# Kernel tuning notes

Measured on AMD Instinct MI355X. Metric: run time of the kernel, lower is better.

Reference implementation:

```python
import jax, jax.numpy as jnp
from jax import lax
import numpy as np

HEAD_SIZE = 64
D_MIX = 32
D_DECAY = 64
D_GATE = 64


def setup_inputs() -> dict:
    key = jax.random.key(0)
    B, T, C = 4, 2048, 1024
    H = C // HEAD_SIZE
    ks = jax.random.split(key, 24)
    n = lambda i, shape, s=1.0: (jax.random.normal(ks[i], shape, dtype=jnp.float32) * s)
    return {
        "x": n(0, (B, T, C)),
        "maa_x": n(1, (C,), 0.1), "maa_w": n(2, (C,), 0.1), "maa_k": n(3, (C,), 0.1),
        "maa_v": n(4, (C,), 0.1), "maa_r": n(5, (C,), 0.1), "maa_g": n(6, (C,), 0.1),
        "maa_w1": n(7, (C, 5 * D_MIX), 0.01), "maa_w2": n(8, (5, D_MIX, C), 0.01),
        "Wr": n(9, (C, C), C ** -0.5), "Wk": n(10, (C, C), C ** -0.5),
        "Wv": n(11, (C, C), C ** -0.5), "Wo": n(12, (C, C), C ** -0.5),
        "gate_w1": n(13, (C, D_GATE), 0.01), "gate_w2": n(14, (D_GATE, C), 0.01),
        "time_decay": n(15, (C,), 1.0) - 4.0,
        "decay_w1": n(16, (C, D_DECAY), 0.01), "decay_w2": n(17, (D_DECAY, C), 0.01),
        "u": n(18, (H, HEAD_SIZE), 0.1),
        "ln_g": jnp.ones((C,), jnp.float32), "ln_b": jnp.zeros((C,), jnp.float32),
    }


def _wkv6(r, k, v, w, u):
    # r,k,v: [B,T,C]; w: decay (already exp(-exp(.))) [B,T,C]; u: [H,N]
    B, T, C = r.shape
    N = HEAD_SIZE
    H = C // N
    to_h = lambda a: a.reshape(B, T, H, N).transpose(1, 0, 2, 3)  # [T,B,H,N]
    rT, kT, vT, wT = map(to_h, (r, k, v, w))

    def step(S, inp):  # S: [B,H,N,N] (key_dim i x value_dim j)
        rt, kt, vt, wt = inp
        kv = kt[..., :, None] * vt[..., None, :]            # [B,H,N,N]
        y = jnp.einsum('bhi,bhij->bhj', rt, S + u[None, :, :, None] * kv)
        S = wt[..., None] * S + kv
        return S, y

    S0 = jnp.zeros((B, H, N, N), r.dtype)
    _, y = lax.scan(step, S0, (rT, kT, vT, wT))
    return y.transpose(1, 0, 2, 3).reshape(B, T, C)


def reference(x, maa_x, maa_w, maa_k, maa_v, maa_r, maa_g, maa_w1, maa_w2,
              Wr, Wk, Wv, Wo, gate_w1, gate_w2, time_decay, decay_w1, decay_w2,
              u, ln_g, ln_b):
    B, T, C = x.shape
    H, N = C // HEAD_SIZE, HEAD_SIZE
    # time shift: prepend zero row, drop last (ZeroPad2d((0,0,1,-1)))
    xx = jnp.concatenate([jnp.zeros_like(x[:, :1]), x[:, :-1]], axis=1) - x
    xxx = x + xx * maa_x
    lora = jnp.tanh(xxx @ maa_w1).reshape(B, T, 5, D_MIX)
    m = jnp.einsum('btfd,fdc->fbtc', lora, maa_w2)  # [5,B,T,C]
    mw, mk, mv, mr, mg = m[0], m[1], m[2], m[3], m[4]
    xw = x + xx * (maa_w + mw)
    xk = x + xx * (maa_k + mk)
    xv = x + xx * (maa_v + mv)
    xr = x + xx * (maa_r + mr)
    xg = x + xx * (maa_g + mg)
    r = xr @ Wr
    k = xk @ Wk
    v = xv @ Wv
    g = jnp.tanh(xg @ gate_w1) @ gate_w2
    w = time_decay + jnp.tanh(xw @ decay_w1) @ decay_w2
    wdec = jnp.exp(-jnp.exp(w))  # decay applied inside the CUDA kernel
    y = _wkv6(r, k, v, wdec, u)
    # GroupNorm over heads, eps = 1e-5 * HEAD_SIZE_DIVISOR**2 = 6.4e-4
    yh = y.reshape(B, T, H, N)
    mu = yh.mean(-1, keepdims=True)
    var = yh.var(-1, keepdims=True)
    yn = ((yh - mu) / jnp.sqrt(var + 6.4e-4)).reshape(B, T, C) * ln_g + ln_b
    return (yn * g) @ Wo
```

## Files before the change

kernel.cpp:

```cpp
#include <hip/hip_runtime.h>
#include <hip/hip_bf16.h>
#include <stdint.h>

typedef __hip_bfloat16 bf16;
typedef __attribute__((ext_vector_type(8))) short bf16x8;
typedef __attribute__((ext_vector_type(4))) float f32x4;

#define CC 1024
#define TT 2048
#define BB 4
#define BT 8192
#define HH 16
#define NN 64

#define MFMA(a, b, c) __builtin_amdgcn_mfma_f32_16x16x32_bf16(a, b, c, 0, 0, 0)

#define GLD(g, l) __builtin_amdgcn_global_load_lds( \
    (const __attribute__((address_space(1))) void*)(g), \
    (__attribute__((address_space(3))) void*)(l), 16, 0, 0)

__device__ __forceinline__ short f2bs(float f) {
    bf16 h = __float2bfloat16(f);
    return *reinterpret_cast<short*>(&h);
}
__device__ __forceinline__ float bs2f(short s) {
    bf16 h = *reinterpret_cast<bf16*>(&s);
    return __bfloat162float(h);
}

template <typename EPI>
__device__ __forceinline__ void gemm128(short* As, short* Bs,
                                        const bf16* __restrict__ A, int lda,
                                        const bf16* __restrict__ Bt, int ldb,
                                        int kiters, int m0, int n0, EPI epi)
{
    const int tid = threadIdx.x;
    const int l   = tid & 63, wv = tid >> 6;
    const int wm  = wv >> 1, wn = wv & 1;
    const int q   = l >> 4, lr = l & 15;
    const int row = tid & 127, kg1 = tid >> 7;

    f32x4 acc[4][4] = {};

    const bf16* ga = A  + (size_t)(m0 + row) * lda + kg1 * 8;
    const bf16* gb = Bt + (size_t)(n0 + row) * ldb + kg1 * 8;
    short* la1 = As + tid * 8;
    short* la2 = As + (tid + 256) * 8;
    short* lb1 = Bs + tid * 8;
    short* lb2 = Bs + (tid + 256) * 8;

    for (int kb = 0; kb < kiters; ++kb) {
        __syncthreads();
        const bf16* gak = ga + kb * 32;
        const bf16* gbk = gb + kb * 32;
        GLD(gak,      la1);
        GLD(gak + 16, la2);
        GLD(gbk,      lb1);
        GLD(gbk + 16, lb2);
        __syncthreads();
        bf16x8 af[4], bfb[4];
#pragma unroll
        for (int mt = 0; mt < 4; ++mt)
            af[mt] = *(const bf16x8*)(As + (q * 128 + wm * 64 + mt * 16 + lr) * 8);
#pragma unroll
        for (int nt = 0; nt < 4; ++nt)
            bfb[nt] = *(const bf16x8*)(Bs + (q * 128 + wn * 64 + nt * 16 + lr) * 8);
#pragma unroll
        for (int mt = 0; mt < 4; ++mt)
#pragma unroll
            for (int nt = 0; nt < 4; ++nt)
                acc[mt][nt] = MFMA(af[mt], bfb[nt], acc[mt][nt]);
    }
#pragma unroll
    for (int mt = 0; mt < 4; ++mt)
#pragma unroll
        for (int nt = 0; nt < 4; ++nt)
#pragma unroll
            for (int rr = 0; rr < 4; ++rr)
                epi(m0 + wm * 64 + mt * 16 + q * 4 + rr,
                    n0 + wn * 64 + nt * 16 + lr, acc[mt][nt][rr]);
}

template <typename EPI>
__device__ __forceinline__ void gemm128k64(short* As, short* Bs,
                                           const bf16* __restrict__ A, int lda,
                                           const bf16* __restrict__ Bt, int ldb,
                                           int kiters, int m0, int n0, EPI epi)
{
    const int tid = threadIdx.x;
    const int l   = tid & 63, wv = tid >> 6;
    const int wm  = wv >> 1, wn = wv & 1;
    const int q   = l >> 4, lr = l & 15;
    const int row = tid & 127, kg1 = tid >> 7;

    f32x4 acc[4][4] = {};

    const bf16* ga = A  + (size_t)(m0 + row) * lda + kg1 * 8;
    const bf16* gb = Bt + (size_t)(n0 + row) * ldb + kg1 * 8;

    auto stage = [&](int kb, int u) {
        const bf16* gak = ga + kb * 64;
        const bf16* gbk = gb + kb * 64;
        short* la = As + u * 8192 + tid * 8;
        short* lb = Bs + u * 8192 + tid * 8;
        GLD(gak,      la);
        GLD(gak + 16, la + 2048);
        GLD(gak + 32, la + 4096);
        GLD(gak + 48, la + 6144);
        GLD(gbk,      lb);
        GLD(gbk + 16, lb + 2048);
        GLD(gbk + 32, lb + 4096);
        GLD(gbk + 48, lb + 6144);
    };

    __syncthreads();
    stage(0, 0);
    __syncthreads();
    for (int kb = 0; kb < kiters; ++kb) {
        const int cur = kb & 1;
        if (kb + 1 < kiters) stage(kb + 1, cur ^ 1);
        const short* Ac = As + cur * 8192;
        const short* Bc = Bs + cur * 8192;
        bf16x8 af[2][4], bfb[2][4];
#pragma unroll
        for (int hh = 0; hh < 2; ++hh) {
#pragma unroll
            for (int mt = 0; mt < 4; ++mt)
                af[hh][mt] = *(const bf16x8*)(Ac +
                    ((q + hh * 4) * 128 + wm * 64 + mt * 16 + lr) * 8);
#pragma unroll
            for (int nt = 0; nt < 4; ++nt)
                bfb[hh][nt] = *(const bf16x8*)(Bc +
                    ((q + hh * 4) * 128 + wn * 64 + nt * 16 + lr) * 8);
        }
        __builtin_amdgcn_s_setprio(1);
#pragma unroll
        for (int mt = 0; mt < 4; ++mt)
#pragma unroll
            for (int nt = 0; nt < 4; ++nt) {
                acc[mt][nt] = MFMA(af[0][mt], bfb[0][nt], acc[mt][nt]);
                acc[mt][nt] = MFMA(af[1][mt], bfb[1][nt], acc[mt][nt]);
            }
        __builtin_amdgcn_s_setprio(0);
        __syncthreads();
    }
#pragma unroll
    for (int mt = 0; mt < 4; ++mt)
#pragma unroll
        for (int nt = 0; nt < 4; ++nt)
#pragma unroll
            for (int rr = 0; rr < 4; ++rr)
                epi(m0 + wm * 64 + mt * 16 + q * 4 + rr,
                    n0 + wn * 64 + nt * 16 + lr, acc[mt][nt][rr]);
}

template <typename EPI>
__device__ __forceinline__ void gemm256(short* As, short* Bs,
                                        const bf16* __restrict__ A, int lda,
                                        const bf16* __restrict__ Bt, int ldb,
                                        int kiters, int m0, int n0, EPI epi)
{
    const int tid = threadIdx.x;
    const int l   = tid & 63, wv = tid >> 6;
    const int wm  = wv >> 2, wn = wv & 3;
    const int q   = l >> 4, lr = l & 15;
    const int row = tid & 255, kg = tid >> 8;

    f32x4 acc[8][4] = {};

    const bf16* ga = A  + (size_t)(m0 + row) * lda + kg * 8;
    const bf16* gb = Bt + (size_t)(n0 + row) * ldb + kg * 8;

    auto stage = [&](int kb, int u) {
        const bf16* gak = ga + kb * 64;
        const bf16* gbk = gb + kb * 64;
        short* la = As + u * 16384 + tid * 8;
        short* lb = Bs + u * 16384 + tid * 8;
        GLD(gak,      la);
        GLD(gak + 16, la + 4096);
        GLD(gak + 32, la + 8192);
        GLD(gak + 48, la + 12288);
        GLD(gbk,      lb);
        GLD(gbk + 16, lb + 4096);
        GLD(gbk + 32, lb + 8192);
        GLD(gbk + 48, lb + 12288);
    };

    __syncthreads();
    stage(0, 0);
    __syncthreads();
    for (int kb = 0; kb < kiters; ++kb) {
        const int cur = kb & 1;
        if (kb + 1 < kiters) stage(kb + 1, cur ^ 1);
        const short* Ac = As + cur * 16384;
        const short* Bc = Bs + cur * 16384;
#pragma unroll
        for (int hh = 0; hh < 2; ++hh) {
            bf16x8 af[8], bfb[4];
#pragma unroll
            for (int mt = 0; mt < 8; ++mt)
                af[mt] = *(const bf16x8*)(Ac +
                    ((q + hh * 4) * 256 + wm * 128 + mt * 16 + lr) * 8);
#pragma unroll
            for (int nt = 0; nt < 4; ++nt)
                bfb[nt] = *(const bf16x8*)(Bc +
                    ((q + hh * 4) * 256 + wn * 64 + nt * 16 + lr) * 8);
            __builtin_amdgcn_s_setprio(1);
#pragma unroll
            for (int mt = 0; mt < 8; ++mt)
#pragma unroll
                for (int nt = 0; nt < 4; ++nt)
                    acc[mt][nt] = MFMA(af[mt], bfb[nt], acc[mt][nt]);
            __builtin_amdgcn_s_setprio(0);
        }
        __syncthreads();
    }
#pragma unroll
    for (int mt = 0; mt < 8; ++mt)
#pragma unroll
        for (int nt = 0; nt < 4; ++nt)
#pragma unroll
            for (int rr = 0; rr < 4; ++rr)
                epi(m0 + wm * 128 + mt * 16 + q * 4 + rr,
                    n0 + wn * 64 + nt * 16 + lr, acc[mt][nt][rr]);
}

template <typename EPI>
__device__ __forceinline__ void gemmHid(short* As, short* Bs,
                                        const bf16* __restrict__ A, int lda,
                                        const bf16* __restrict__ Bt, int ldb,
                                        int kiters, int m0, EPI epi)
{
    const int tid = threadIdx.x;
    const int l   = tid & 63, wv = tid >> 6;
    const int q   = l >> 4, lr = l & 15;
    const int row = tid & 255, kg = tid >> 8;
    const int row64 = tid & 63, kg8 = tid >> 6;

    f32x4 acc[2][4] = {};

    const bf16* ga = A  + (size_t)(m0 + row) * lda + kg * 8;
    const bf16* gb = Bt + (size_t)row64 * ldb + kg8 * 8;

    auto stage = [&](int kb, int u) {
        const bf16* gak = ga + kb * 64;
        short* la = As + u * 16384 + tid * 8;
        GLD(gak,      la);
        GLD(gak + 16, la + 4096);
        GLD(gak + 32, la + 8192);
        GLD(gak + 48, la + 12288);
        GLD(gb + kb * 64, Bs + u * 4096 + tid * 8);
    };

    __syncthreads();
    stage(0, 0);
    __syncthreads();
    for (int kb = 0; kb < kiters; ++kb) {
        const int cur = kb & 1;
        if (kb + 1 < kiters) stage(kb + 1, cur ^ 1);
        const short* Ac = As + cur * 16384;
        const short* Bc = Bs + cur * 4096;
        bf16x8 af[2][2], bfb[2][4];
#pragma unroll
        for (int hh = 0; hh < 2; ++hh) {
#pragma unroll
            for (int mt = 0; mt < 2; ++mt)
                af[hh][mt] = *(const bf16x8*)(Ac +
                    ((q + hh * 4) * 256 + wv * 32 + mt * 16 + lr) * 8);
#pragma unroll
            for (int nt = 0; nt < 4; ++nt)
                bfb[hh][nt] = *(const bf16x8*)(Bc +
                    ((q + hh * 4) * 64 + nt * 16 + lr) * 8);
        }
#pragma unroll
        for (int mt = 0; mt < 2; ++mt)
#pragma unroll
            for (int nt = 0; nt < 4; ++nt) {
                acc[mt][nt] = MFMA(af[0][mt], bfb[0][nt], acc[mt][nt]);
                acc[mt][nt] = MFMA(af[1][mt], bfb[1][nt], acc[mt][nt]);
            }
        __syncthreads();
    }
#pragma unroll
    for (int mt = 0; mt < 2; ++mt)
#pragma unroll
        for (int nt = 0; nt < 4; ++nt)
#pragma unroll
            for (int rr = 0; rr < 4; ++rr)
                epi(m0 + wv * 32 + mt * 16 + q * 4 + rr,
                    nt * 16 + lr, acc[mt][nt][rr]);
}

__global__ __launch_bounds__(256) void k_prep_all(
    const float* __restrict__ Wr, const float* __restrict__ Wk,
    const float* __restrict__ Wv, const float* __restrict__ Wo,
    const float* __restrict__ maa_w1, const float* __restrict__ gate_w1,
    const float* __restrict__ decay_w1, const float* __restrict__ gate_w2,
    const float* __restrict__ decay_w2, const float* __restrict__ maa_w2,
    const float* __restrict__ mw, const float* __restrict__ mk,
    const float* __restrict__ mv, const float* __restrict__ mr,
    const float* __restrict__ mg, const float* __restrict__ x,
    const float* __restrict__ maa_x,
    bf16* __restrict__ WT3, bf16* __restrict__ WoT, bf16* __restrict__ w1T,
    bf16* __restrict__ w1T2, bf16* __restrict__ w2T2, bf16* __restrict__ w2T5,
    float* __restrict__ maas, bf16* __restrict__ xxx,
    bf16* __restrict__ xb, bf16* __restrict__ xxb)
{
    __shared__ float tile[32][33];
    int idx = blockIdx.x;
    if (idx >= 4900) {
        size_t i = ((size_t)(idx - 4900) * 256 + threadIdx.x) * 4;
        int cc = i & (CC - 1);
        int t  = (i >> 10) & (TT - 1);
        float4 xm = *(const float4*)(x + i);
        float4 xp = t ? *(const float4*)(x + i - CC)
                      : make_float4(0.f, 0.f, 0.f, 0.f);
        float4 ax = *(const float4*)(maa_x + cc);
        float xxv[4] = {xp.x - xm.x, xp.y - xm.y, xp.z - xm.z, xp.w - xm.w};
        float xmv[4] = {xm.x, xm.y, xm.z, xm.w};
        float axv[4] = {ax.x, ax.y, ax.z, ax.w};
#pragma unroll
        for (int e = 0; e < 4; ++e) {
            xb[i + e]  = __float2bfloat16(xmv[e]);
            xxb[i + e] = __float2bfloat16(xxv[e]);
            xxx[i + e] = __float2bfloat16(xmv[e] + xxv[e] * axv[e]);
        }
        return;
    }
    const float* src; bf16* dst; int rows, cols_in, tx_;
    if (idx < 4096) {
        int s = idx >> 10; idx &= 1023;
        src = (s == 0) ? Wr : (s == 1) ? Wk : (s == 2) ? Wv : Wo;
        dst = (s == 3) ? WoT : WT3 + (size_t)s * CC * CC;
        rows = CC; cols_in = CC; tx_ = 32;
    } else if (idx < 4352) { idx -= 4096; src = maa_w1;  dst = w1T;  rows = CC; cols_in = 160; tx_ = 8; }
    else if (idx < 4480)   { idx -= 4352; src = gate_w1; dst = w1T2; rows = CC; cols_in = 64;  tx_ = 4; }
    else if (idx < 4608)   { idx -= 4480; src = decay_w1; dst = w1T2 + 128 * CC; rows = CC; cols_in = 64; tx_ = 4; }
    else if (idx < 4672)   { idx -= 4608; src = gate_w2;  dst = w2T2;           rows = 64; cols_in = CC; tx_ = 32; }
    else if (idx < 4736)   { idx -= 4672; src = decay_w2; dst = w2T2 + CC * 64; rows = 64; cols_in = CC; tx_ = 32; }
    else if (idx < 4896)   { idx -= 4736; int f = idx >> 5; idx &= 31;
                             src = maa_w2 + (size_t)f * 32 * CC;
                             dst = w2T5 + (size_t)f * CC * 32; rows = 32; cols_in = CC; tx_ = 32; }
    else {
        int i = (idx - 4896) * 256 + threadIdx.x;
        if (i < CC) {
            maas[i]          = mw[i];
            maas[CC + i]     = mk[i];
            maas[2 * CC + i] = mv[i];
            maas[3 * CC + i] = mr[i];
            maas[4 * CC + i] = mg[i];
        }
        return;
    }
    int bx = idx % tx_, by = idx / tx_;
    int c0 = bx * 32, r0 = by * 32;
    int tx = threadIdx.x & 31, ty = threadIdx.x >> 5;
    for (int i = ty; i < 32; i += 8) {
        int cc2 = c0 + tx;
        tile[i][tx] = (cc2 < cols_in) ? src[(size_t)(r0 + i) * cols_in + cc2] : 0.f;
    }
    __syncthreads();
    for (int i = ty; i < 32; i += 8)
        dst[(size_t)(c0 + i) * rows + r0 + tx] = __float2bfloat16(tile[tx][i]);
}

__global__ __launch_bounds__(256) void g_lora(const bf16* __restrict__ xxx,
                                              const bf16* __restrict__ w1T,
                                              bf16* __restrict__ L)
{
    __shared__ __align__(16) short lds[8192];
    int m0 = blockIdx.x * 128, n0 = blockIdx.y * 128;
    gemm128(lds, lds + 4096, xxx, CC, w1T, CC, CC / 32, m0, n0,
            [&](int m, int n, float v) {
                if (n < 160) L[(size_t)m * 160 + n] = __float2bfloat16(tanhf(v));
            });
}

__global__ __launch_bounds__(256) void g_xvar(const bf16* __restrict__ L,
                                              const bf16* __restrict__ w2T,
                                              const float* __restrict__ maas,
                                              const bf16* __restrict__ xb,
                                              const bf16* __restrict__ xxb,
                                              bf16* __restrict__ xvars)
{
    __shared__ __align__(16) short lds[8192];
    int m0 = blockIdx.x * 128, n0 = blockIdx.y * 128;
    for (int f = 0; f < 5; ++f) {
        const bf16* A  = L + f * 32;
        const bf16* Bt = w2T + (size_t)f * CC * 32;
        const float* maa = maas + f * CC;
        bf16* out = xvars + (size_t)f * BT * CC;
        gemm128(lds, lds + 4096, A, 160, Bt, 32, 1, m0, n0,
                [&](int m, int n, float v) {
                    float xm = __bfloat162float(xb[(size_t)m * CC + n]);
                    float xx = __bfloat162float(xxb[(size_t)m * CC + n]);
                    out[(size_t)m * CC + n] =
                        __float2bfloat16(xm + xx * (maa[n] + v));
                });
    }
}

__global__ __launch_bounds__(512) void g_rkv5(const bf16* __restrict__ xvars,
                                              const bf16* __restrict__ WT,
                                              const bf16* __restrict__ w1T2,
                                              bf16* __restrict__ rkv,
                                              bf16* __restrict__ hid)
{
    __shared__ __align__(16) short lds[65536];
    int bid = blockIdx.x;
    if (bid < 384) {
        int swz = (bid & 7) * 48 + (bid >> 3);
        int z  = swz >> 7;
        int r2 = swz & 127;
        int n0 = (r2 >> 5) * 256;
        int m0 = (r2 & 31) * 256;
        int f = (z == 0) ? 3 : z;
        const bf16* A  = xvars + (size_t)f * BT * CC;
        const bf16* Bt = WT + (size_t)z * CC * CC;
        bf16* out = rkv + (size_t)z * BT * CC;
        gemm256(lds, lds + 32768, A, CC, Bt, CC, CC / 64, m0, n0,
                [&](int m, int n, float v) {
                    out[(size_t)m * CC + n] = __float2bfloat16(v);
                });
    } else {
        int hb = bid - 384;
        int zz = hb >> 5, mi = hb & 31;
        const bf16* A  = xvars + (size_t)(zz == 0 ? 4 : 0) * BT * CC;
        const bf16* Bt = w1T2 + (size_t)zz * 128 * CC;
        bf16* out = hid + (size_t)zz * BT * 64;
        gemmHid(lds, lds + 32768, A, CC, Bt, CC, CC / 64, mi * 256,
                [&](int m, int n, float v) {
                    out[(size_t)m * 64 + n] = __float2bfloat16(tanhf(v));
                });
    }
}

__global__ __launch_bounds__(256) void k_wkv_p1(const bf16* __restrict__ r,
                                                const bf16* __restrict__ kk,
                                                const bf16* __restrict__ vv,
                                                const bf16* __restrict__ hidW,
                                                const bf16* __restrict__ w2d,
                                                const float* __restrict__ td,
                                                const float* __restrict__ u,
                                                bf16* __restrict__ y,
                                                bf16* __restrict__ RTg,
                                                short* __restrict__ Mg,
                                                float* __restrict__ plg)
{
    constexpr int PW = 65, PB = 72;
    __shared__ __align__(16) char smem[16640 + 3 * 9216 + 768];
    float* LW = (float*)smem;
    short* VT = (short*)smem;
    short* RT = (short*)(smem + 16640);
    short* KT = (short*)(smem + 16640 + 9216);
    short* AT = KT;
    short* KH = (short*)(smem + 16640 + 2 * 9216);
    short* HT = KT;
    short* WD = KH;
    float* SU = (float*)(smem + 16640 + 3 * 9216);
    float* SD = SU + 64;

    const int tid = threadIdx.x;
    const int lane = tid & 63, wq = tid >> 6;
    const int row = tid >> 2, g = tid & 3, j0 = g * 16;
    const int l15 = lane & 15, q = lane >> 4;
    const int bh = blockIdx.x >> 5, c = blockIdx.x & 31;
    const int b = bh >> 4, h = bh & 15;
    const size_t base = (size_t)b * TT * CC + (size_t)h * NN;
    const int t0 = c * 64;
    const int bt0 = b * TT + t0;
    const size_t cb = (size_t)blockIdx.x * 4096;

    if (tid < 64) SU[tid] = u[h * NN + tid];

#pragma unroll
    for (int rnd = 0; rnd < 2; ++rnd) {
        int ee = rnd * 256 + tid;
        int rw = ee >> 3, c8 = (ee & 7) * 8;
        *(bf16x8*)(HT + rw * PB + c8) =
            *(const bf16x8*)(hidW + (size_t)(bt0 + rw) * 64 + c8);
        *(bf16x8*)(WD + rw * PB + c8) =
            *(const bf16x8*)(w2d + (size_t)(h * 64 + rw) * 64 + c8);
    }
    const size_t gb = base + (size_t)(t0 + row) * CC + j0;
    bf16x8 r0 = *(const bf16x8*)(r + gb),  r1 = *(const bf16x8*)(r + gb + 8);
    bf16x8 k0 = *(const bf16x8*)(kk + gb), k1 = *(const bf16x8*)(kk + gb + 8);
    bf16x8 v0 = *(const bf16x8*)(vv + gb), v1 = *(const bf16x8*)(vv + gb + 8);
    float tdv[4];
#pragma unroll
    for (int ct = 0; ct < 4; ++ct) tdv[ct] = td[h * 64 + ct * 16 + l15];
    __syncthreads();
    {
        bf16x8 aH0 = *(const bf16x8*)(HT + (wq * 16 + l15) * PB + q * 8);
        bf16x8 aH1 = *(const bf16x8*)(HT + (wq * 16 + l15) * PB + q * 8 + 32);
        f32x4 lwa[4] = {};
#pragma unroll
        for (int ct = 0; ct < 4; ++ct) {
            bf16x8 bW0 = *(const bf16x8*)(WD + (ct * 16 + l15) * PB + q * 8);
            bf16x8 bW1 = *(const bf16x8*)(WD + (ct * 16 + l15) * PB + q * 8 + 32);
            lwa[ct] = MFMA(aH0, bW0, lwa[ct]);
            lwa[ct] = MFMA(aH1, bW1, lwa[ct]);
        }
#pragma unroll
        for (int ct = 0; ct < 4; ++ct)
#pragma unroll
            for (int rr = 0; rr < 4; ++rr) {
                int t = wq * 16 + q * 4 + rr, j = ct * 16 + l15;
                LW[t * PW + j] = -expf(tdv[ct] + lwa[ct][rr]);
            }
    }
    __syncthreads();
    for (int jj = 0; jj < 16; ++jj) {
        int j = wq * 16 + jj;
        float xv = LW[lane * PW + j];
#pragma unroll
        for (int d = 1; d < 64; d <<= 1) {
            float t2 = __shfl_up(xv, d);
            if (lane >= d) xv += t2;
        }
        LW[lane * PW + j] = xv;
    }
    __syncthreads();
    float rF[16], kF[16];
#pragma unroll
    for (int c2 = 0; c2 < 8; ++c2) {
        rF[c2] = bs2f(r0[c2]); rF[8 + c2] = bs2f(r1[c2]);
        kF[c2] = bs2f(k0[c2]); kF[8 + c2] = bs2f(k1[c2]);
    }
    float cwp[16], cwm[16], cwL[16];
#pragma unroll
    for (int c2 = 0; c2 < 16; ++c2) {
        cwp[c2] = LW[row * PW + j0 + c2];
        cwm[c2] = row ? LW[(row - 1) * PW + j0 + c2] : 0.f;
        cwL[c2] = LW[63 * PW + j0 + c2];
    }
    bf16x8 w0, w1;
#pragma unroll
    for (int c2 = 0; c2 < 8; ++c2) {
        w0[c2] = f2bs(rF[c2] * expf(cwm[c2]));
        w1[c2] = f2bs(rF[8 + c2] * expf(cwm[8 + c2]));
    }
    *(bf16x8*)(RT + row * PB + j0)     = w0;
    *(bf16x8*)(RT + row * PB + j0 + 8) = w1;
    *(bf16x8*)((short*)RTg + cb + row * 64 + j0)     = w0;
    *(bf16x8*)((short*)RTg + cb + row * 64 + j0 + 8) = w1;
#pragma unroll
    for (int c2 = 0; c2 < 8; ++c2) {
        w0[c2] = f2bs(kF[c2] * expf(-cwp[c2]));
        w1[c2] = f2bs(kF[8 + c2] * expf(-cwp[8 + c2]));
    }
    *(bf16x8*)(KT + row * PB + j0)     = w0;
    *(bf16x8*)(KT + row * PB + j0 + 8) = w1;
#pragma unroll
    for (int c2 = 0; c2 < 16; ++c2)
        KH[(j0 + c2) * PB + row] = f2bs(kF[c2] * expf(cwL[c2] - cwp[c2]));
    if (tid < 64) plg[(size_t)blockIdx.x * 64 + tid] = expf(LW[63 * PW + tid]);
    float dpart = 0.f;
#pragma unroll
    for (int c2 = 0; c2 < 16; ++c2)
        dpart = fmaf(rF[c2] * kF[c2], SU[j0 + c2], dpart);
    dpart += __shfl_xor(dpart, 1);
    dpart += __shfl_xor(dpart, 2);
    if (g == 0) SD[row] = dpart;
    __syncthreads();
#pragma unroll
    for (int c2 = 0; c2 < 8; ++c2) {
        VT[(j0 + c2) * PB + row]     = v0[c2];
        VT[(j0 + 8 + c2) * PB + row] = v1[c2];
    }
    bf16x8 aF0 = *(const bf16x8*)(RT + (wq * 16 + l15) * PB + q * 8);
    bf16x8 aF1 = *(const bf16x8*)(RT + (wq * 16 + l15) * PB + q * 8 + 32);
    f32x4 Am[4] = {};
#pragma unroll
    for (int ct = 0; ct < 4; ++ct) {
        bf16x8 bF0 = *(const bf16x8*)(KT + (ct * 16 + l15) * PB + q * 8);
        bf16x8 bF1 = *(const bf16x8*)(KT + (ct * 16 + l15) * PB + q * 8 + 32);
        Am[ct] = MFMA(aF0, bF0, Am[ct]);
        Am[ct] = MFMA(aF1, bF1, Am[ct]);
    }
    __syncthreads();
#pragma unroll
    for (int ct = 0; ct < 4; ++ct)
#pragma unroll
        for (int rr = 0; rr < 4; ++rr) {
            int s = wq * 16 + q * 4 + rr, p = ct * 16 + l15;
            float vA = Am[ct][rr];
            vA = (p > s) ? 0.f : (p == s ? SD[s] : vA);
            AT[s * PB + p] = f2bs(vA);
        }
    __syncthreads();
    f32x4 Y[4] = {}, M[4] = {};
    bf16x8 aA0 = *(const bf16x8*)(AT + (wq * 16 + l15) * PB + q * 8);
    bf16x8 aA1 = *(const bf16x8*)(AT + (wq * 16 + l15) * PB + q * 8 + 32);
    bf16x8 aV0 = *(const bf16x8*)(VT + (wq * 16 + l15) * PB + q * 8);
    bf16x8 aV1 = *(const bf16x8*)(VT + (wq * 16 + l15) * PB + q * 8 + 32);
#pragma unroll
    for (int ct = 0; ct < 4; ++ct) {
        bf16x8 bV0 = *(const bf16x8*)(VT + (ct * 16 + l15) * PB + q * 8);
        bf16x8 bV1 = *(const bf16x8*)(VT + (ct * 16 + l15) * PB + q * 8 + 32);
        Y[ct] = MFMA(aA0, bV0, Y[ct]);
        Y[ct] = MFMA(aA1, bV1, Y[ct]);
        bf16x8 bK0 = *(const bf16x8*)(KH + (ct * 16 + l15) * PB + q * 8);
        bf16x8 bK1 = *(const bf16x8*)(KH + (ct * 16 + l15) * PB + q * 8 + 32);
        M[ct] = MFMA(aV0, bK0, M[ct]);
        M[ct] = MFMA(aV1, bK1, M[ct]);
    }
#pragma unroll
    for (int ct = 0; ct < 4; ++ct)
#pragma unroll
        for (int rr = 0; rr < 4; ++rr) {
            int s = wq * 16 + q * 4 + rr;
            y[base + (size_t)(t0 + s) * CC + ct * 16 + l15] =
                __float2bfloat16(Y[ct][rr]);
            Mg[cb + (size_t)s * 64 + ct * 16 + l15] = f2bs(M[ct][rr]);
        }
}

__global__ __launch_bounds__(256) void k_wkv_p2(const short* __restrict__ Mg,
                                                const float* __restrict__ plg,
                                                bf16* __restrict__ Sg)
{
    int bh = blockIdx.x >> 4, part = blockIdx.x & 15;
    int i = part * 4 + (threadIdx.x >> 6), j = threadIdx.x & 63;
    float S = 0.f;
    size_t eb = (size_t)bh * 32 * 4096 + (size_t)i * 64 + j;
    size_t pb = (size_t)bh * 32 * 64 + j;
    for (int c = 0; c < 32; ++c) {
        Sg[eb + (size_t)c * 4096] = __float2bfloat16(S);
        S = plg[pb + (size_t)c * 64] * S + bs2f(Mg[eb + (size_t)c * 4096]);
    }
}

__global__ __launch_bounds__(256) void k_wkv_p3(const bf16* __restrict__ RTg,
                                                const bf16* __restrict__ Sg,
                                                const bf16* __restrict__ y,
                                                const bf16* __restrict__ hidG,
                                                const bf16* __restrict__ w2g,
                                                const float* __restrict__ ln_g,
                                                const float* __restrict__ ln_b,
                                                bf16* __restrict__ A2)
{
    constexpr int PB = 72;
    __shared__ __align__(16) short BufA[64 * PB], BufB[64 * PB];
    const int tid = threadIdx.x;
    const int lane = tid & 63, wq = tid >> 6;
    const int l15 = lane & 15, q = lane >> 4;
    const int bh = blockIdx.x >> 5, c = blockIdx.x & 31;
    const int b = bh >> 4, h = bh & 15;
    const int t0 = c * 64;
    const int bt0 = b * TT + t0;
    const size_t cb = (size_t)blockIdx.x * 4096;

#pragma unroll
    for (int rnd = 0; rnd < 2; ++rnd) {
        int ee = rnd * 256 + tid;
        int rw = ee >> 3, c8 = (ee & 7) * 8;
        *(bf16x8*)(BufA + rw * PB + c8) =
            *(const bf16x8*)(hidG + (size_t)(bt0 + rw) * 64 + c8);
        *(bf16x8*)(BufB + rw * PB + c8) =
            *(const bf16x8*)(w2g + (size_t)(h * 64 + rw) * 64 + c8);
    }
    __syncthreads();
    f32x4 G[4] = {};
    {
        bf16x8 aH0 = *(const bf16x8*)(BufA + (wq * 16 + l15) * PB + q * 8);
        bf16x8 aH1 = *(const bf16x8*)(BufA + (wq * 16 + l15) * PB + q * 8 + 32);
#pragma unroll
        for (int ct = 0; ct < 4; ++ct) {
            bf16x8 bW0 = *(const bf16x8*)(BufB + (ct * 16 + l15) * PB + q * 8);
            bf16x8 bW1 = *(const bf16x8*)(BufB + (ct * 16 + l15) * PB + q * 8 + 32);
            G[ct] = MFMA(aH0, bW0, G[ct]);
            G[ct] = MFMA(aH1, bW1, G[ct]);
        }
    }
    __syncthreads();
#pragma unroll
    for (int rnd = 0; rnd < 2; ++rnd) {
        int ee = rnd * 256 + tid;
        int rw = ee >> 3, c8 = (ee & 7) * 8;
        *(bf16x8*)(BufA + rw * PB + c8) =
            *(const bf16x8*)((const short*)RTg + cb + rw * 64 + c8);
        *(bf16x8*)(BufB + rw * PB + c8) =
            *(const bf16x8*)((const short*)Sg + cb + rw * 64 + c8);
    }
    __syncthreads();

    f32x4 Yc[4];
#pragma unroll
    for (int ct = 0; ct < 4; ++ct)
#pragma unroll
        for (int rr = 0; rr < 4; ++rr) {
            int s = wq * 16 + q * 4 + rr;
            Yc[ct][rr] = __bfloat162float(
                y[((size_t)bt0 + s) * CC + h * NN + ct * 16 + l15]);
        }
    bf16x8 aF0 = *(const bf16x8*)(BufA + (wq * 16 + l15) * PB + q * 8);
    bf16x8 aF1 = *(const bf16x8*)(BufA + (wq * 16 + l15) * PB + q * 8 + 32);
#pragma unroll
    for (int ct = 0; ct < 4; ++ct) {
        bf16x8 bS0 = *(const bf16x8*)(BufB + (ct * 16 + l15) * PB + q * 8);
        bf16x8 bS1 = *(const bf16x8*)(BufB + (ct * 16 + l15) * PB + q * 8 + 32);
        Yc[ct] = MFMA(aF0, bS0, Yc[ct]);
        Yc[ct] = MFMA(aF1, bS1, Yc[ct]);
    }
#pragma unroll
    for (int rr = 0; rr < 4; ++rr) {
        float s1 = 0.f, s2 = 0.f;
#pragma unroll
        for (int ct = 0; ct < 4; ++ct) {
            float vA = Yc[ct][rr];
            s1 += vA; s2 += vA * vA;
        }
#pragma unroll
        for (int o = 1; o < 16; o <<= 1) {
            s1 += __shfl_xor(s1, o);
            s2 += __shfl_xor(s2, o);
        }
        float mu  = s1 * (1.f / 64.f);
        float var = s2 * (1.f / 64.f) - mu * mu;
        float rstd = rsqrtf(var + 6.4e-4f);
        int s = wq * 16 + q * 4 + rr;
        size_t mrow = ((size_t)bt0 + s) * CC;
#pragma unroll
        for (int ct = 0; ct < 4; ++ct) {
            int ch = h * NN + ct * 16 + l15;
            float yn = (Yc[ct][rr] - mu) * rstd;
            float out = (yn * ln_g[ch] + ln_b[ch]) * G[ct][rr];
            A2[mrow + ch] = __float2bfloat16(out);
        }
    }
}

__global__ __launch_bounds__(256) void g_out(const bf16* __restrict__ A2,
                                             const bf16* __restrict__ WoT,
                                             float* __restrict__ out)
{
    __shared__ __align__(16) short lds[32768];
    int m0 = blockIdx.x * 128, n0 = blockIdx.y * 128;
    gemm128k64(lds, lds + 16384, A2, CC, WoT, CC, CC / 64, m0, n0,
               [&](int m, int n, float v) { out[(size_t)m * CC + n] = v; });
}

extern "C" void kernel_launch(void* const* d_in, const int* in_sizes, int n_in,
                              void* d_out, int out_size, void* d_ws, size_t ws_size,
                              hipStream_t stream)
{
    const float* x        = (const float*)d_in[0];
    const float* maa_x    = (const float*)d_in[1];
    const float* maa_w    = (const float*)d_in[2];
    const float* maa_k    = (const float*)d_in[3];
    const float* maa_v    = (const float*)d_in[4];
    const float* maa_r    = (const float*)d_in[5];
    const float* maa_g    = (const float*)d_in[6];
    const float* maa_w1   = (const float*)d_in[7];
    const float* maa_w2   = (const float*)d_in[8];
    const float* Wr       = (const float*)d_in[9];
    const float* Wk       = (const float*)d_in[10];
    const float* Wv       = (const float*)d_in[11];
    const float* Wo       = (const float*)d_in[12];
    const float* gate_w1  = (const float*)d_in[13];
    const float* gate_w2  = (const float*)d_in[14];
    const float* time_dec = (const float*)d_in[15];
    const float* decay_w1 = (const float*)d_in[16];
    const float* decay_w2 = (const float*)d_in[17];
    const float* u        = (const float*)d_in[18];
    const float* ln_g     = (const float*)d_in[19];
    const float* ln_b     = (const float*)d_in[20];

    size_t off = 0;
    auto alloc = [&](size_t bytes) {
        off = (off + 255) & ~(size_t)255;
        void* p = (char*)d_ws + off;
        off += bytes;
        return p;
    };
    bf16*  WT3   = (bf16*) alloc(3ull * CC * CC * 2);
    bf16*  WoT   = (bf16*) alloc((size_t)CC * CC * 2);
    bf16*  w1T   = (bf16*) alloc(256ull * CC * 2);
    bf16*  w1T2  = (bf16*) alloc(2ull * 128 * CC * 2);
    bf16*  w2T2  = (bf16*) alloc(2ull * CC * 64 * 2);
    bf16*  w2T5  = (bf16*) alloc(5ull * CC * 32 * 2);
    float* maas  = (float*)alloc(5ull * CC * 4);
    char* bufA = (char*)alloc((size_t)BT * CC * 2);
    bf16* xxxbf = (bf16*)bufA;
    bf16* A2    = (bf16*)bufA;
    char* bufB = (char*)alloc((size_t)BT * 160 * 2);
    bf16* Lbf  = (bf16*)bufB;
    bf16* hid  = (bf16*)bufB;
    char* bufC = (char*)alloc(5ull * BT * CC * 2);
    bf16*  xvars = (bf16*)bufC;
    bf16*  ybuf  = (bf16*)bufC;
    bf16*  RTg   = (bf16*)(bufC + (size_t)BT * CC * 2);
    bf16*  rkv  = (bf16*)alloc(3ull * BT * CC * 2);
    bf16*  Sg   = rkv;
    bf16*  xb   = (bf16*) alloc((size_t)BT * CC * 2);
    bf16*  xxb  = (bf16*) alloc((size_t)BT * CC * 2);
    short* Mg   = (short*)alloc(64ull * 32 * 4096 * 2);
    float* plg  = (float*)alloc(64ull * 32 * 64 * 4);

    k_prep_all<<<dim3(13092), 256, 0, stream>>>(
        Wr, Wk, Wv, Wo, maa_w1, gate_w1, decay_w1, gate_w2, decay_w2, maa_w2,
        maa_w, maa_k, maa_v, maa_r, maa_g, x, maa_x,
        WT3, WoT, w1T, w1T2, w2T2, w2T5, maas, xxxbf, xb, xxb);

    g_lora<<<dim3(64, 2), 256, 0, stream>>>(xxxbf, w1T, Lbf);
    g_xvar<<<dim3(64, 8), 256, 0, stream>>>(Lbf, w2T5, maas, xb, xxb, xvars);
    g_rkv5<<<dim3(448), 512, 0, stream>>>(xvars, WT3, w1T2, rkv, hid);
    k_wkv_p1<<<dim3(2048), 256, 0, stream>>>(rkv, rkv + (size_t)BT * CC,
                                             rkv + 2ull * BT * CC,
                                             hid + (size_t)BT * 64,
                                             w2T2 + CC * 64,
                                             time_dec, u, ybuf, RTg, Mg, plg);
    k_wkv_p2<<<dim3(1024), 256, 0, stream>>>(Mg, plg, Sg);
    k_wkv_p3<<<dim3(2048), 256, 0, stream>>>(RTg, Sg, ybuf,
                                             hid,
                                             w2T2,
                                             ln_g, ln_b, A2);
    g_out<<<dim3(64, 8), 256, 0, stream>>>(A2, WoT, (float*)d_out);
}
```

Baseline: 401.9 us.

## Store GEMM operands in pre-tiled blocked layout for contiguous LDS staging

The producers of xvars and the transposed Wr/Wk/Wv weights now write them in a 256-row x 64-k blocked layout. The gemm256 and gemmHid staging loads then read one contiguous 32KB tile per k-step instead of strided row segments. This is meant to make the global-to-LDS loads fully coalesced and cut address arithmetic. In exchange, the xvar epilogue and the weight transpose now do scattered stores, and every consumer of xvars must understand the blocked layout.

```diff
diff --git a/kernel.cpp b/kernel.cpp
--- a/kernel.cpp
+++ b/kernel.cpp
@@ -26,6 +26,11 @@
 __device__ __forceinline__ float bs2f(short s) {
     bf16 h = *reinterpret_cast<bf16*>(&s);
     return __bfloat162float(h);
+}
+
+__device__ __forceinline__ size_t blk_idx(int m, int k, int ktiles) {
+    return ((size_t)(m >> 8) * ktiles + (k >> 6)) * 16384
+         + ((k >> 3) & 7) * 2048 + (m & 255) * 8 + (k & 7);
 }
 
 template <typename EPI>
@@ -156,34 +161,33 @@
 
 template <typename EPI>
 __device__ __forceinline__ void gemm256(short* As, short* Bs,
-                                        const bf16* __restrict__ A, int lda,
-                                        const bf16* __restrict__ Bt, int ldb,
+                                        const bf16* __restrict__ A,
+                                        const bf16* __restrict__ Bt,
                                         int kiters, int m0, int n0, EPI epi)
 {
     const int tid = threadIdx.x;
     const int l   = tid & 63, wv = tid >> 6;
     const int wm  = wv >> 2, wn = wv & 3;
     const int q   = l >> 4, lr = l & 15;
-    const int row = tid & 255, kg = tid >> 8;
 
     f32x4 acc[8][4] = {};
 
-    const bf16* ga = A  + (size_t)(m0 + row) * lda + kg * 8;
-    const bf16* gb = Bt + (size_t)(n0 + row) * ldb + kg * 8;
+    const bf16* ga = A  + (size_t)(m0 >> 8) * 16 * 16384 + tid * 8;
+    const bf16* gb = Bt + (size_t)(n0 >> 8) * 16 * 16384 + tid * 8;
 
     auto stage = [&](int kb, int u) {
-        const bf16* gak = ga + kb * 64;
-        const bf16* gbk = gb + kb * 64;
+        const bf16* gak = ga + (size_t)kb * 16384;
+        const bf16* gbk = gb + (size_t)kb * 16384;
         short* la = As + u * 16384 + tid * 8;
         short* lb = Bs + u * 16384 + tid * 8;
-        GLD(gak,      la);
-        GLD(gak + 16, la + 4096);
-        GLD(gak + 32, la + 8192);
-        GLD(gak + 48, la + 12288);
-        GLD(gbk,      lb);
-        GLD(gbk + 16, lb + 4096);
-        GLD(gbk + 32, lb + 8192);
-        GLD(gbk + 48, lb + 12288);
+        GLD(gak,         la);
+        GLD(gak + 4096,  la + 4096);
+        GLD(gak + 8192,  la + 8192);
+        GLD(gak + 12288, la + 12288);
+        GLD(gbk,         lb);
+        GLD(gbk + 4096,  lb + 4096);
+        GLD(gbk + 8192,  lb + 8192);
+        GLD(gbk + 12288, lb + 12288);
     };
 
     __syncthreads();
@@ -227,28 +231,27 @@
 
 template <typename EPI>
 __device__ __forceinline__ void gemmHid(short* As, short* Bs,
-                                        const bf16* __restrict__ A, int lda,
+                                        const bf16* __restrict__ A,
                                         const bf16* __restrict__ Bt, int ldb,
                                         int kiters, int m0, EPI epi)
 {
     const int tid = threadIdx.x;
     const int l   = tid & 63, wv = tid >> 6;
     const int q   = l >> 4, lr = l & 15;
-    const int row = tid & 255, kg = tid >> 8;
     const int row64 = tid & 63, kg8 = tid >> 6;
 
     f32x4 acc[2][4] = {};
 
-    const bf16* ga = A  + (size_t)(m0 + row) * lda + kg * 8;
+    const bf16* ga = A + (size_t)(m0 >> 8) * 16 * 16384 + tid * 8;
     const bf16* gb = Bt + (size_t)row64 * ldb + kg8 * 8;
 
     auto stage = [&](int kb, int u) {
-        const bf16* gak = ga + kb * 64;
+        const bf16* gak = ga + (size_t)kb * 16384;
         short* la = As + u * 16384 + tid * 8;
-        GLD(gak,      la);
-        GLD(gak + 16, la + 4096);
-        GLD(gak + 32, la + 8192);
-        GLD(gak + 48, la + 12288);
+        GLD(gak,         la);
+        GLD(gak + 4096,  la + 4096);
+        GLD(gak + 8192,  la + 8192);
+        GLD(gak + 12288, la + 12288);
         GLD(gb + kb * 64, Bs + u * 4096 + tid * 8);
     };
 
@@ -328,10 +331,12 @@
         return;
     }
     const float* src; bf16* dst; int rows, cols_in, tx_;
+    bool blocked = false;
     if (idx < 4096) {
         int s = idx >> 10; idx &= 1023;
         src = (s == 0) ? Wr : (s == 1) ? Wk : (s == 2) ? Wv : Wo;
         dst = (s == 3) ? WoT : WT3 + (size_t)s * CC * CC;
+        blocked = (s != 3);
         rows = CC; cols_in = CC; tx_ = 32;
     } else if (idx < 4352) { idx -= 4096; src = maa_w1;  dst = w1T;  rows = CC; cols_in = 160; tx_ = 8; }
     else if (idx < 4480)   { idx -= 4352; src = gate_w1; dst = w1T2; rows = CC; cols_in = 64;  tx_ = 4; }
@@ -360,8 +365,15 @@
         tile[i][tx] = (cc2 < cols_in) ? src[(size_t)(r0 + i) * cols_in + cc2] : 0.f;
     }
     __syncthreads();
-    for (int i = ty; i < 32; i += 8)
-        dst[(size_t)(c0 + i) * rows + r0 + tx] = __float2bfloat16(tile[tx][i]);
+    if (blocked) {
+        for (int i = ty; i < 32; i += 8) {
+            int R = c0 + i, C = r0 + tx;
+            dst[blk_idx(R, C, 16)] = __float2bfloat16(tile[tx][i]);
+        }
+    } else {
+        for (int i = ty; i < 32; i += 8)
+            dst[(size_t)(c0 + i) * rows + r0 + tx] = __float2bfloat16(tile[tx][i]);
+    }
 }
 
 __global__ __launch_bounds__(256) void g_lora(const bf16* __restrict__ xxx,
@@ -394,7 +406,7 @@
                 [&](int m, int n, float v) {
                     float xm = __bfloat162float(xb[(size_t)m * CC + n]);
                     float xx = __bfloat162float(xxb[(size_t)m * CC + n]);
-                    out[(size_t)m * CC + n] =
+                    out[blk_idx(m, n, 16)] =
                         __float2bfloat16(xm + xx * (maa[n] + v));
                 });
     }
@@ -418,7 +430,7 @@
         const bf16* A  = xvars + (size_t)f * BT * CC;
         const bf16* Bt = WT + (size_t)z * CC * CC;
         bf16* out = rkv + (size_t)z * BT * CC;
-        gemm256(lds, lds + 32768, A, CC, Bt, CC, CC / 64, m0, n0,
+        gemm256(lds, lds + 32768, A, Bt, CC / 64, m0, n0,
                 [&](int m, int n, float v) {
                     out[(size_t)m * CC + n] = __float2bfloat16(v);
                 });
@@ -428,7 +440,7 @@
         const bf16* A  = xvars + (size_t)(zz == 0 ? 4 : 0) * BT * CC;
         const bf16* Bt = w1T2 + (size_t)zz * 128 * CC;
         bf16* out = hid + (size_t)zz * BT * 64;
-        gemmHid(lds, lds + 32768, A, CC, Bt, CC, CC / 64, mi * 256,
+        gemmHid(lds, lds + 32768, A, Bt, CC, CC / 64, mi * 256,
                 [&](int m, int n, float v) {
                     out[(size_t)m * 64 + n] = __float2bfloat16(tanhf(v));
                 });
```

Result: faster. 380.8 us (-5.3%).
